# Kernel optimization log

Hardware: AMD Instinct MI355X
Metric: run time of the kernel (lower is better)

The kernel has to match this reference:

```python
import jax, jax.numpy as jnp
import numpy as np

N, F_IN, F_HID, F_OUT = 16384, 128, 128, 64
EDGE_P = 0.001  # Bernoulli edge probability -> avg degree ~16


def _sage_conv(x, mask_t, deg_inv, Wl, b, Wr):
    # PyG SAGEConv (mean aggr): out = lin_l(mean_agg) + lin_r(x); lin_l has bias.
    agg = (mask_t @ x) * deg_inv[:, None]  # [N, Fin] mean over incoming edges
    return agg @ Wl.T + b + x @ Wr.T


def setup_inputs() -> dict:
    key = jax.random.key(0)
    ks = jax.random.split(key, 12)
    x = jax.random.normal(ks[0], (N, F_IN), dtype=jnp.float32)
    adj = (jax.random.uniform(ks[1], (N, N)) < EDGE_P).astype(jnp.float32)

    def lin(k, fo, fi):
        s = 1.0 / np.sqrt(fi)
        return jax.random.uniform(k, (fo, fi), jnp.float32, -s, s)

    dims = [(F_HID, F_IN), (F_HID, F_HID), (F_OUT, F_HID)]
    params = {}
    for i, (fo, fi) in enumerate(dims):
        params[f"Wl{i}"] = lin(ks[2 + 3 * i], fo, fi)
        params[f"b{i}"] = jnp.zeros((fo,), jnp.float32)
        params[f"Wr{i}"] = lin(ks[3 + 3 * i], fo, fi)
    return {"x": x, "adj": adj, **params}


def reference(x, adj, Wl0, b0, Wr0, Wl1, b1, Wr1, Wl2, b2, Wr2):
    # edge (r, c): adj[r, c] != 0, source r -> target c (PyG convention).
    mask = (adj != 0).astype(x.dtype)
    deg = mask.sum(axis=0)                      # incoming degree per target node
    deg_inv = jnp.where(deg > 0, 1.0 / jnp.maximum(deg, 1.0), 0.0)
    mask_t = mask.T                             # [target, source]
    # Dropout layers are identity in eval mode.
    h = jax.nn.relu(_sage_conv(x, mask_t, deg_inv, Wl0, b0, Wr0))
    h = jax.nn.relu(_sage_conv(h, mask_t, deg_inv, Wl1, b1, Wr1))
    out = _sage_conv(h, mask_t, deg_inv, Wl2, b2, Wr2)
    return out
```

## Files before the change

kernel.cpp:

```cpp
#include <hip/hip_runtime.h>


#define NN 16384
#define FIN 128
#define CAP (1 << 19)
#define LBUF 1024

typedef int iv4 __attribute__((ext_vector_type(4)));

#define OFF_CNT   0u
#define OFF_DEG   256u
#define OFF_OFFS  65792u
#define OFF_CUR   131584u
#define OFF_DINV  197120u
#define OFF_PAIRS 262656u
#define OFF_ESRC  (262656u + 8u * CAP)
#define OFF_WT0   (OFF_ESRC + 4u * CAP)
#define OFF_WT1   (OFF_WT0 + 131072u)
#define OFF_WT2   (OFF_WT1 + 131072u)
#define OFF_H1    (OFF_WT2 + 65536u)
#define OFF_H2    (OFF_H1 + 4u * NN * FIN)

__global__ void k_wt(const float* __restrict__ Wl0, const float* __restrict__ Wr0,
                     const float* __restrict__ Wl1, const float* __restrict__ Wr1,
                     const float* __restrict__ Wl2, const float* __restrict__ Wr2,
                     float* __restrict__ wt0, float* __restrict__ wt1,
                     float* __restrict__ wt2) {
    int g = blockIdx.x * 256 + threadIdx.x;
    if (g < 32768) {
        int k = g >> 7, o = g & 127;
        wt0[g] = (k < 128) ? Wl0[o * 128 + k] : Wr0[o * 128 + (k - 128)];
    } else if (g < 65536) {
        int gg = g - 32768;
        int k = gg >> 7, o = gg & 127;
        wt1[gg] = (k < 128) ? Wl1[o * 128 + k] : Wr1[o * 128 + (k - 128)];
    } else if (g < 81920) {
        int gg = g - 65536;
        int k = gg >> 6, o = gg & 63;
        wt2[gg] = (k < 128) ? Wl2[o * 128 + k] : Wr2[o * 128 + (k - 128)];
    }
}

__device__ __forceinline__ void emit_hits(iv4 v, int idx4, int* __restrict__ deg,
                                          unsigned int* lcnt,
                                          unsigned long long* lbuf) {
    if ((v.x | v.y | v.z | v.w) == 0) return;
    int base = idx4 << 2;
    int s = base >> 14;
    int t = base & (NN - 1);
    int w[4] = {v.x, v.y, v.z, v.w};
    #pragma unroll
    for (int k = 0; k < 4; ++k) {
        if (w[k] != 0) {
            atomicAdd(&deg[t + k], 1);
            unsigned int idx = atomicAdd(lcnt, 1u);
            if (idx < LBUF)
                lbuf[idx] = ((unsigned long long)s << 32) | (unsigned)(t + k);
        }
    }
}

__global__ __launch_bounds__(256) void k_count(
    const iv4* __restrict__ adj4, int* __restrict__ deg,
    unsigned int* __restrict__ cnt, unsigned long long* __restrict__ pairs) {
    __shared__ unsigned int lcnt;
    __shared__ unsigned int lbase;
    __shared__ unsigned long long lbuf[LBUF];
    const int tid = threadIdx.x;
    if (tid == 0) lcnt = 0;
    __syncthreads();

    const int stride = 2048 * 256;
    int i = blockIdx.x * 256 + tid;
    #pragma unroll 1
    for (int n = 0; n < 64; ++n, i += 2 * stride) {
        iv4 a = __builtin_nontemporal_load(&adj4[i]);
        iv4 b = __builtin_nontemporal_load(&adj4[i + stride]);
        emit_hits(a, i, deg, &lcnt, lbuf);
        emit_hits(b, i + stride, deg, &lcnt, lbuf);
    }
    __syncthreads();
    unsigned int total = lcnt;
    if (total > LBUF) total = LBUF;
    if (tid == 0) lbase = atomicAdd(cnt, total);
    __syncthreads();
    unsigned int bb = lbase;
    for (unsigned int j = tid; j < total; j += 256)
        if (bb + j < CAP) pairs[bb + j] = lbuf[j];
}

__global__ __launch_bounds__(1024) void k_scan(
    const int* __restrict__ deg, int* __restrict__ offs,
    int* __restrict__ cur, float* __restrict__ dinv) {
    __shared__ int ps[1024];
    int tid = threadIdx.x;
    int base = tid * 16;
    int local = 0;
    #pragma unroll
    for (int j = 0; j < 16; ++j) local += deg[base + j];
    ps[tid] = local;
    __syncthreads();
    for (int ofs = 1; ofs < 1024; ofs <<= 1) {
        int v = (tid >= ofs) ? ps[tid - ofs] : 0;
        __syncthreads();
        ps[tid] += v;
        __syncthreads();
    }
    int run = ps[tid] - local;
    #pragma unroll
    for (int j = 0; j < 16; ++j) {
        int d = deg[base + j];
        offs[base + j] = run;
        cur[base + j] = run;
        dinv[base + j] = d > 0 ? 1.0f / (float)d : 0.0f;
        run += d;
    }
    if (tid == 1023) offs[NN] = run;
}

__global__ void k_bin(const unsigned long long* __restrict__ pairs,
                      const unsigned int* __restrict__ cnt,
                      int* __restrict__ cur, int* __restrict__ esrc) {
    unsigned int total = *cnt;
    if (total > CAP) total = CAP;
    unsigned int stride = gridDim.x * blockDim.x;
    for (unsigned int i = blockIdx.x * blockDim.x + threadIdx.x; i < total; i += stride) {
        unsigned long long p = pairs[i];
        int s = (int)(p >> 32);
        int t = (int)(p & 0xFFFFFFFFull);
        int pos = atomicAdd(&cur[t], 1);
        esrc[pos] = s;
    }
}

template <int FOUT, bool RELU>
__global__ __launch_bounds__(256) void k_layer(
    const float4* __restrict__ hin,
    float4* __restrict__ hout,
    const int* __restrict__ esrc, const int* __restrict__ offs,
    const float* __restrict__ dinv,
    const float4* __restrict__ Wt4,
    const float4* __restrict__ b4)
{
    constexpr int S4 = 66;
    __shared__ float4 z[16 * S4];
    const int tid = threadIdx.x;
    const int nodeBase = blockIdx.x * 16;

    #pragma unroll
    for (int r = 0; r < 2; ++r) {
        int g = tid + 256 * r;
        int n = g >> 5, j = g & 31;
        z[n * S4 + 32 + j] = hin[(nodeBase + n) * 32 + j];
    }

    {
        const int nl = tid >> 4;
        const int q = tid & 15;
        const int node = nodeBase + nl;
        const int e0 = offs[node], e1 = offs[node + 1];
        float4 acc0 = make_float4(0.f, 0.f, 0.f, 0.f);
        float4 acc1 = make_float4(0.f, 0.f, 0.f, 0.f);
        for (int e = e0; e < e1; ++e) {
            int s = esrc[e];
            const float4* row = hin + s * 32;
            float4 v0 = row[q];
            float4 v1 = row[q + 16];
            acc0.x += v0.x; acc0.y += v0.y; acc0.z += v0.z; acc0.w += v0.w;
            acc1.x += v1.x; acc1.y += v1.y; acc1.z += v1.z; acc1.w += v1.w;
        }
        const float di = dinv[node];
        acc0.x *= di; acc0.y *= di; acc0.z *= di; acc0.w *= di;
        acc1.x *= di; acc1.y *= di; acc1.z *= di; acc1.w *= di;
        z[nl * S4 + q] = acc0;
        z[nl * S4 + q + 16] = acc1;
    }
    __syncthreads();

    constexpr int TO = FOUT / 4;
    constexpr int TN = 256 / TO;
    constexpr int NPT = 16 / TN;
    const int to = tid % TO;
    const int tn = tid / TO;

    float acc[NPT][4];
    #pragma unroll
    for (int m = 0; m < NPT; ++m)
        #pragma unroll
        for (int r = 0; r < 4; ++r) acc[m][r] = 0.f;

    #pragma unroll 4
    for (int k4 = 0; k4 < 64; ++k4) {
        float4 w0 = Wt4[(4 * k4 + 0) * TO + to];
        float4 w1 = Wt4[(4 * k4 + 1) * TO + to];
        float4 w2 = Wt4[(4 * k4 + 2) * TO + to];
        float4 w3 = Wt4[(4 * k4 + 3) * TO + to];
        #pragma unroll
        for (int m = 0; m < NPT; ++m) {
            float4 a = z[(tn * NPT + m) * S4 + k4];
            acc[m][0] += a.x * w0.x + a.y * w1.x + a.z * w2.x + a.w * w3.x;
            acc[m][1] += a.x * w0.y + a.y * w1.y + a.z * w2.y + a.w * w3.y;
            acc[m][2] += a.x * w0.z + a.y * w1.z + a.z * w2.z + a.w * w3.z;
            acc[m][3] += a.x * w0.w + a.y * w1.w + a.z * w2.w + a.w * w3.w;
        }
    }

    float4 bb = b4[to];
    #pragma unroll
    for (int m = 0; m < NPT; ++m) {
        float4 o;
        o.x = acc[m][0] + bb.x;
        o.y = acc[m][1] + bb.y;
        o.z = acc[m][2] + bb.z;
        o.w = acc[m][3] + bb.w;
        if (RELU) {
            o.x = fmaxf(o.x, 0.f); o.y = fmaxf(o.y, 0.f);
            o.z = fmaxf(o.z, 0.f); o.w = fmaxf(o.w, 0.f);
        }
        hout[(nodeBase + tn * NPT + m) * (FOUT / 4) + to] = o;
    }
}

extern "C" void kernel_launch(void* const* d_in, const int* in_sizes, int n_in,
                              void* d_out, int out_size, void* d_ws, size_t ws_size,
                              hipStream_t stream) {
    const float* x = (const float*)d_in[0];
    const iv4* adj4 = (const iv4*)d_in[1];
    const float* Wl0 = (const float*)d_in[2];
    const float4* b0 = (const float4*)d_in[3];
    const float* Wr0 = (const float*)d_in[4];
    const float* Wl1 = (const float*)d_in[5];
    const float4* b1 = (const float4*)d_in[6];
    const float* Wr1 = (const float*)d_in[7];
    const float* Wl2 = (const float*)d_in[8];
    const float4* b2 = (const float4*)d_in[9];
    const float* Wr2 = (const float*)d_in[10];

    char* ws = (char*)d_ws;
    unsigned int* cnt = (unsigned int*)(ws + OFF_CNT);
    int* deg = (int*)(ws + OFF_DEG);
    int* offs = (int*)(ws + OFF_OFFS);
    int* cur = (int*)(ws + OFF_CUR);
    float* dinv = (float*)(ws + OFF_DINV);
    unsigned long long* pairs = (unsigned long long*)(ws + OFF_PAIRS);
    int* esrc = (int*)(ws + OFF_ESRC);
    float* wt0 = (float*)(ws + OFF_WT0);
    float* wt1 = (float*)(ws + OFF_WT1);
    float* wt2 = (float*)(ws + OFF_WT2);
    float4* h1 = (float4*)(ws + OFF_H1);
    float4* h2 = (float4*)(ws + OFF_H2);

    (void)hipMemsetAsync(ws, 0, OFF_OFFS, stream);

    k_wt<<<320, 256, 0, stream>>>(Wl0, Wr0, Wl1, Wr1, Wl2, Wr2, wt0, wt1, wt2);
    k_count<<<2048, 256, 0, stream>>>(adj4, deg, cnt, pairs);
    k_scan<<<1, 1024, 0, stream>>>(deg, offs, cur, dinv);
    k_bin<<<512, 256, 0, stream>>>(pairs, cnt, cur, esrc);
    k_layer<128, true><<<NN / 16, 256, 0, stream>>>(
        (const float4*)x, h1, esrc, offs, dinv, (const float4*)wt0, b0);
    k_layer<128, true><<<NN / 16, 256, 0, stream>>>(
        (const float4*)h1, h2, esrc, offs, dinv, (const float4*)wt1, b1);
    k_layer<64, false><<<NN / 16, 256, 0, stream>>>(
        (const float4*)h2, (float4*)d_out, esrc, offs, dinv, (const float4*)wt2, b2);
}
```

Before: 1.535 ms.

## Use one warp per node for gather and GEMM, unroll adjacency scan

The layer kernel now handles 8 nodes per block with 32 threads per node. Each thread gathers one float4 per neighbor row, with neighbor loads unrolled by four to keep more loads in flight. The dense transform assigns one node per thread group, with float2 outputs for the 64-wide layer, and twice as many blocks are launched. The adjacency count kernel also loads four vectors per iteration instead of two. The trade-off is less weight reuse per block, since each weight load now serves one node instead of several, which raises weight traffic from cache.

```diff
diff --git a/kernel.cpp b/kernel.cpp
--- a/kernel.cpp
+++ b/kernel.cpp
@@ -73,11 +73,15 @@
     const int stride = 2048 * 256;
     int i = blockIdx.x * 256 + tid;
     #pragma unroll 1
-    for (int n = 0; n < 64; ++n, i += 2 * stride) {
+    for (int n = 0; n < 32; ++n, i += 4 * stride) {
         iv4 a = __builtin_nontemporal_load(&adj4[i]);
         iv4 b = __builtin_nontemporal_load(&adj4[i + stride]);
+        iv4 c = __builtin_nontemporal_load(&adj4[i + 2 * stride]);
+        iv4 d = __builtin_nontemporal_load(&adj4[i + 3 * stride]);
         emit_hits(a, i, deg, &lcnt, lbuf);
         emit_hits(b, i + stride, deg, &lcnt, lbuf);
+        emit_hits(c, i + 2 * stride, deg, &lcnt, lbuf);
+        emit_hits(d, i + 3 * stride, deg, &lcnt, lbuf);
     }
     __syncthreads();
     unsigned int total = lcnt;
@@ -136,88 +140,92 @@
 template <int FOUT, bool RELU>
 __global__ __launch_bounds__(256) void k_layer(
     const float4* __restrict__ hin,
-    float4* __restrict__ hout,
+    float* __restrict__ hout,
     const int* __restrict__ esrc, const int* __restrict__ offs,
     const float* __restrict__ dinv,
     const float4* __restrict__ Wt4,
-    const float4* __restrict__ b4)
+    const float* __restrict__ bias)
 {
     constexpr int S4 = 66;
-    __shared__ float4 z[16 * S4];
+    __shared__ float4 z[8 * S4];
     const int tid = threadIdx.x;
-    const int nodeBase = blockIdx.x * 16;
-
-    #pragma unroll
-    for (int r = 0; r < 2; ++r) {
-        int g = tid + 256 * r;
-        int n = g >> 5, j = g & 31;
-        z[n * S4 + 32 + j] = hin[(nodeBase + n) * 32 + j];
-    }
+    const int nodeBase = blockIdx.x * 8;
+    const int nl = tid >> 5;
+    const int q = tid & 31;
+
+    z[nl * S4 + 32 + q] = hin[(nodeBase + nl) * 32 + q];
 
     {
-        const int nl = tid >> 4;
-        const int q = tid & 15;
         const int node = nodeBase + nl;
         const int e0 = offs[node], e1 = offs[node + 1];
-        float4 acc0 = make_float4(0.f, 0.f, 0.f, 0.f);
-        float4 acc1 = make_float4(0.f, 0.f, 0.f, 0.f);
-        for (int e = e0; e < e1; ++e) {
-            int s = esrc[e];
-            const float4* row = hin + s * 32;
-            float4 v0 = row[q];
-            float4 v1 = row[q + 16];
-            acc0.x += v0.x; acc0.y += v0.y; acc0.z += v0.z; acc0.w += v0.w;
-            acc1.x += v1.x; acc1.y += v1.y; acc1.z += v1.z; acc1.w += v1.w;
+        float4 acc = make_float4(0.f, 0.f, 0.f, 0.f);
+        int e = e0;
+        for (; e + 4 <= e1; e += 4) {
+            int s0 = esrc[e], s1 = esrc[e + 1], s2 = esrc[e + 2], s3 = esrc[e + 3];
+            float4 v0 = hin[s0 * 32 + q];
+            float4 v1 = hin[s1 * 32 + q];
+            float4 v2 = hin[s2 * 32 + q];
+            float4 v3 = hin[s3 * 32 + q];
+            acc.x += v0.x + v1.x + v2.x + v3.x;
+            acc.y += v0.y + v1.y + v2.y + v3.y;
+            acc.z += v0.z + v1.z + v2.z + v3.z;
+            acc.w += v0.w + v1.w + v2.w + v3.w;
+        }
+        for (; e < e1; ++e) {
+            float4 v = hin[esrc[e] * 32 + q];
+            acc.x += v.x; acc.y += v.y; acc.z += v.z; acc.w += v.w;
         }
         const float di = dinv[node];
-        acc0.x *= di; acc0.y *= di; acc0.z *= di; acc0.w *= di;
-        acc1.x *= di; acc1.y *= di; acc1.z *= di; acc1.w *= di;
-        z[nl * S4 + q] = acc0;
-        z[nl * S4 + q + 16] = acc1;
-    }
-    __syncthreads();
-
-    constexpr int TO = FOUT / 4;
-    constexpr int TN = 256 / TO;
-    constexpr int NPT = 16 / TN;
-    const int to = tid % TO;
-    const int tn = tid / TO;
-
-    float acc[NPT][4];
-    #pragma unroll
-    for (int m = 0; m < NPT; ++m)
-        #pragma unroll
-        for (int r = 0; r < 4; ++r) acc[m][r] = 0.f;
-
-    #pragma unroll 4
-    for (int k4 = 0; k4 < 64; ++k4) {
-        float4 w0 = Wt4[(4 * k4 + 0) * TO + to];
-        float4 w1 = Wt4[(4 * k4 + 1) * TO + to];
-        float4 w2 = Wt4[(4 * k4 + 2) * TO + to];
-        float4 w3 = Wt4[(4 * k4 + 3) * TO + to];
-        #pragma unroll
-        for (int m = 0; m < NPT; ++m) {
-            float4 a = z[(tn * NPT + m) * S4 + k4];
-            acc[m][0] += a.x * w0.x + a.y * w1.x + a.z * w2.x + a.w * w3.x;
-            acc[m][1] += a.x * w0.y + a.y * w1.y + a.z * w2.y + a.w * w3.y;
-            acc[m][2] += a.x * w0.z + a.y * w1.z + a.z * w2.z + a.w * w3.z;
-            acc[m][3] += a.x * w0.w + a.y * w1.w + a.z * w2.w + a.w * w3.w;
-        }
-    }
-
-    float4 bb = b4[to];
-    #pragma unroll
-    for (int m = 0; m < NPT; ++m) {
+        acc.x *= di; acc.y *= di; acc.z *= di; acc.w *= di;
+        z[nl * S4 + q] = acc;
+    }
+    __syncthreads();
+
+    if constexpr (FOUT == 128) {
+        const int to = tid & 31;
+        const int tn = tid >> 5;
+        float4 acc = make_float4(0.f, 0.f, 0.f, 0.f);
+        #pragma unroll 4
+        for (int k4 = 0; k4 < 64; ++k4) {
+            float4 w0 = Wt4[(4 * k4 + 0) * 32 + to];
+            float4 w1 = Wt4[(4 * k4 + 1) * 32 + to];
+            float4 w2 = Wt4[(4 * k4 + 2) * 32 + to];
+            float4 w3 = Wt4[(4 * k4 + 3) * 32 + to];
+            float4 a = z[tn * S4 + k4];
+            acc.x += a.x * w0.x + a.y * w1.x + a.z * w2.x + a.w * w3.x;
+            acc.y += a.x * w0.y + a.y * w1.y + a.z * w2.y + a.w * w3.y;
+            acc.z += a.x * w0.z + a.y * w1.z + a.z * w2.z + a.w * w3.z;
+            acc.w += a.x * w0.w + a.y * w1.w + a.z * w2.w + a.w * w3.w;
+        }
+        const float4 bb = ((const float4*)bias)[to];
         float4 o;
-        o.x = acc[m][0] + bb.x;
-        o.y = acc[m][1] + bb.y;
-        o.z = acc[m][2] + bb.z;
-        o.w = acc[m][3] + bb.w;
+        o.x = acc.x + bb.x; o.y = acc.y + bb.y;
+        o.z = acc.z + bb.z; o.w = acc.w + bb.w;
         if (RELU) {
             o.x = fmaxf(o.x, 0.f); o.y = fmaxf(o.y, 0.f);
             o.z = fmaxf(o.z, 0.f); o.w = fmaxf(o.w, 0.f);
         }
-        hout[(nodeBase + tn * NPT + m) * (FOUT / 4) + to] = o;
+        ((float4*)hout)[(nodeBase + tn) * 32 + to] = o;
+    } else {
+        const float2* Wt2 = (const float2*)Wt4;
+        const int to = tid & 31;
+        const int tn = tid >> 5;
+        float2 acc = make_float2(0.f, 0.f);
+        #pragma unroll 4
+        for (int k4 = 0; k4 < 64; ++k4) {
+            float2 w0 = Wt2[(4 * k4 + 0) * 32 + to];
+            float2 w1 = Wt2[(4 * k4 + 1) * 32 + to];
+            float2 w2 = Wt2[(4 * k4 + 2) * 32 + to];
+            float2 w3 = Wt2[(4 * k4 + 3) * 32 + to];
+            float4 a = z[tn * S4 + k4];
+            acc.x += a.x * w0.x + a.y * w1.x + a.z * w2.x + a.w * w3.x;
+            acc.y += a.x * w0.y + a.y * w1.y + a.z * w2.y + a.w * w3.y;
+        }
+        const float2 bb = ((const float2*)bias)[to];
+        float2 o;
+        o.x = acc.x + bb.x; o.y = acc.y + bb.y;
+        if (RELU) { o.x = fmaxf(o.x, 0.f); o.y = fmaxf(o.y, 0.f); }
+        ((float2*)hout)[(nodeBase + tn) * 32 + to] = o;
     }
 }
 
@@ -227,13 +235,13 @@
     const float* x = (const float*)d_in[0];
     const iv4* adj4 = (const iv4*)d_in[1];
     const float* Wl0 = (const float*)d_in[2];
-    const float4* b0 = (const float4*)d_in[3];
+    const float* b0 = (const float*)d_in[3];
     const float* Wr0 = (const float*)d_in[4];
     const float* Wl1 = (const float*)d_in[5];
-    const float4* b1 = (const float4*)d_in[6];
+    const float* b1 = (const float*)d_in[6];
     const float* Wr1 = (const float*)d_in[7];
     const float* Wl2 = (const float*)d_in[8];
-    const float4* b2 = (const float4*)d_in[9];
+    const float* b2 = (const float*)d_in[9];
     const float* Wr2 = (const float*)d_in[10];
 
     char* ws = (char*)d_ws;
@@ -247,8 +255,8 @@
     float* wt0 = (float*)(ws + OFF_WT0);
     float* wt1 = (float*)(ws + OFF_WT1);
     float* wt2 = (float*)(ws + OFF_WT2);
-    float4* h1 = (float4*)(ws + OFF_H1);
-    float4* h2 = (float4*)(ws + OFF_H2);
+    float* h1 = (float*)(ws + OFF_H1);
+    float* h2 = (float*)(ws + OFF_H2);
 
     (void)hipMemsetAsync(ws, 0, OFF_OFFS, stream);
 
@@ -256,10 +264,10 @@
     k_count<<<2048, 256, 0, stream>>>(adj4, deg, cnt, pairs);
     k_scan<<<1, 1024, 0, stream>>>(deg, offs, cur, dinv);
     k_bin<<<512, 256, 0, stream>>>(pairs, cnt, cur, esrc);
-    k_layer<128, true><<<NN / 16, 256, 0, stream>>>(
+    k_layer<128, true><<<NN / 8, 256, 0, stream>>>(
         (const float4*)x, h1, esrc, offs, dinv, (const float4*)wt0, b0);
-    k_layer<128, true><<<NN / 16, 256, 0, stream>>>(
+    k_layer<128, true><<<NN / 8, 256, 0, stream>>>(
         (const float4*)h1, h2, esrc, offs, dinv, (const float4*)wt1, b1);
-    k_layer<64, false><<<NN / 16, 256, 0, stream>>>(
-        (const float4*)h2, (float4*)d_out, esrc, offs, dinv, (const float4*)wt2, b2);
-}
+    k_layer<64, false><<<NN / 8, 256, 0, stream>>>(
+        (const float4*)h2, (float*)d_out, esrc, offs, dinv, (const float4*)wt2, b2);
+}
```

After: 1.625 ms. +5.9%, slower.
